# Kernel tuning notes

Measured on AMD Instinct MI355X. Metric: run time of the kernel, lower is better.

Reference implementation:

```python
import jax, jax.numpy as jnp
import numpy as np

B, A, D, H = 16384, 16, 512, 512


def setup_inputs() -> dict:
    key = jax.random.key(0)
    ks = jax.random.split(key, 8)
    s = 1.0 / np.sqrt(D)
    sh = 1.0 / np.sqrt(H)
    return {
        "state": jax.random.normal(ks[0], (B, D), jnp.float32),
        "W1": jax.random.normal(ks[1], (A, D, H), jnp.float32) * s,
        "b1": jax.random.normal(ks[2], (A, H), jnp.float32) * s,
        "W2": jax.random.normal(ks[3], (A, H, H), jnp.float32) * sh,
        "b2": jax.random.normal(ks[4], (A, H), jnp.float32) * sh,
        "W3": jax.random.normal(ks[5], (A, H, 1), jnp.float32) * sh,
        "b3": jax.random.normal(ks[6], (A, 1), jnp.float32) * sh,
        "actions": jax.random.randint(ks[7], (B,), 0, A, jnp.int64),
    }


def reference(state, W1, b1, W2, b2, W3, b3, actions):
    # All per-action MLPs applied to every state as grouped/batched GEMMs.
    # h1, h2: [B, A, H]; out: [B, A, n_out]
    h1 = jax.nn.relu(jnp.einsum("bd,adh->bah", state, W1) + b1)
    h2 = jax.nn.relu(jnp.einsum("bah,ahk->bak", h1, W2) + b2)
    out = jnp.einsum("bah,ahk->bak", h2, W3) + b3  # [B, A, 1]
    # Gather the selected action's output per batch element -> [B, n_out]
    return jnp.take_along_axis(out, actions[:, None, None], axis=1)[:, 0, :]
```

## Files before the change

### kernel.cpp

```cpp
#include <hip/hip_runtime.h>
#include <hip/hip_bf16.h>
#include <stdint.h>

typedef __hip_bfloat16 bf16;
typedef float f32x4 __attribute__((ext_vector_type(4)));
typedef short bf16x8 __attribute__((ext_vector_type(8)));

#define NB 16384
#define NA 16
#define ND 512
#define NH 512
#define TR 80

#define W1S_OFF 0u
#define W2S_OFF 8388608u
#define PERM_OFF 16777216u
#define META_OFF 16842752u

__device__ __forceinline__ unsigned short f2b(float x) {
  unsigned int b = __float_as_uint(x);
  return (unsigned short)((b + 0x7FFFu + ((b >> 16) & 1u)) >> 16);
}

__global__ __launch_bounds__(256) void k_prep(const float* __restrict__ W1,
                                              const float* __restrict__ W2,
                                              bf16* __restrict__ W1s,
                                              bf16* __restrict__ W2s,
                                              const int* __restrict__ act,
                                              int* __restrict__ meta,
                                              int* __restrict__ perm) {
  __shared__ union {
    float tile[2][64][65];
    struct { int hist[16][256]; int off16[16]; } m;
  } lds;
  if (blockIdx.x == 512) {
    int t = threadIdx.x;
    int lane = t & 63, wv = t >> 6;
#pragma unroll
    for (int i = 0; i < 16; ++i) lds.m.hist[i][t] = 0;
    __syncthreads();
    for (int j = 0; j < 64; ++j) {
      int a = act[t + (j << 8)] & 15;
      lds.m.hist[a][t]++;
    }
    __syncthreads();
    for (int q = 0; q < 4; ++q) {
      int a = (wv << 2) + q;
      int base = lane << 2;
      int v0 = lds.m.hist[a][base + 0];
      int v1 = lds.m.hist[a][base + 1];
      int v2 = lds.m.hist[a][base + 2];
      int v3 = lds.m.hist[a][base + 3];
      int s = v0 + v1 + v2 + v3;
      int incl = s;
#pragma unroll
      for (int d = 1; d < 64; d <<= 1) {
        int y = __shfl_up(incl, d);
        if (lane >= d) incl += y;
      }
      int excl = incl - s;
      lds.m.hist[a][base + 0] = excl;
      lds.m.hist[a][base + 1] = excl + v0;
      lds.m.hist[a][base + 2] = excl + v0 + v1;
      lds.m.hist[a][base + 3] = excl + v0 + v1 + v2;
      if (lane == 63) lds.m.off16[a] = incl;
    }
    __syncthreads();
    if (t == 0) {
      int o = 0;
      for (int aa = 0; aa < 16; ++aa) {
        int c = lds.m.off16[aa];
        meta[aa] = c;
        meta[16 + aa] = o;
        lds.m.off16[aa] = o;
        o += c;
      }
    }
    __syncthreads();
    for (int j = 0; j < 64; ++j) {
      int idx = t + (j << 8);
      int a = act[idx] & 15;
      int pos = lds.m.off16[a] + lds.m.hist[a][t]++;
      perm[pos] = idx;
    }
    return;
  }
  int bid = blockIdx.x;
  int xcd = bid & 7, q = bid >> 3;
  int t = threadIdx.x;
  int r0 = t >> 2, c0 = (t & 3) << 4;
  int wv = t >> 6, l = t & 63;
  int l15b = l & 15, l4b = l >> 4;

  float4 v[4];
  char* dstb_r[4];
  int td_r[4], th_r[4];
#pragma unroll
  for (int r = 0; r < 4; ++r) {
    int jj = q + (r << 6);
    int mi = jj >> 6;
    int mat = (mi < 2) ? ((xcd << 1) + mi) : (NA + (xcd << 1) + (mi - 2));
    dstb_r[r] = (mat < NA) ? ((char*)W1s + ((size_t)mat << 19))
                           : ((char*)W2s + ((size_t)(mat - NA) << 19));
    int tl = jj & 63;
    td_r[r] = tl >> 3;
    th_r[r] = tl & 7;
  }
  {
    int mi0 = q >> 6;
    const float* src = W1 + (size_t)((xcd << 1) + mi0) * (ND * NH);
    const float* sp = src + (size_t)(td_r[0] * 64 + r0) * NH + th_r[0] * 64 + c0;
    v[0] = ((const float4*)sp)[0];
    v[1] = ((const float4*)sp)[1];
    v[2] = ((const float4*)sp)[2];
    v[3] = ((const float4*)sp)[3];
  }
#pragma unroll
  for (int r = 0; r < 4; ++r) {
    int buf = r & 1;
    float* trp = &lds.tile[buf][r0][c0];
    trp[0] = v[0].x; trp[1] = v[0].y; trp[2] = v[0].z; trp[3] = v[0].w;
    trp[4] = v[1].x; trp[5] = v[1].y; trp[6] = v[1].z; trp[7] = v[1].w;
    trp[8] = v[2].x; trp[9] = v[2].y; trp[10] = v[2].z; trp[11] = v[2].w;
    trp[12] = v[3].x; trp[13] = v[3].y; trp[14] = v[3].z; trp[15] = v[3].w;
    __syncthreads();
    if (r < 3) {
      int jj = q + ((r + 1) << 6);
      int mi = jj >> 6;
      int mat = (mi < 2) ? ((xcd << 1) + mi) : (NA + (xcd << 1) + (mi - 2));
      const float* src = (mat < NA) ? (W1 + (size_t)mat * (ND * NH))
                                    : (W2 + (size_t)(mat - NA) * (ND * NH));
      const float* sp = src + (size_t)(td_r[r + 1] * 64 + r0) * NH + th_r[r + 1] * 64 + c0;
      v[0] = ((const float4*)sp)[0];
      v[1] = ((const float4*)sp)[1];
      v[2] = ((const float4*)sp)[2];
      v[3] = ((const float4*)sp)[3];
    }
#pragma unroll
    for (int kc = 0; kc < 2; ++kc) {
      union { unsigned short us[8]; uint4 qd; } u;
#pragma unroll
      for (int i = 0; i < 8; ++i)
        u.us[i] = f2b(lds.tile[buf][kc * 32 + l4b * 8 + i][wv * 16 + l15b]);
      int hb = th_r[r] * 4 + wv;
      int kb = td_r[r] * 2 + kc;
      *(uint4*)(dstb_r[r] + ((size_t)(hb * 16 + kb) << 10) + (l << 4)) = u.qd;
    }
  }
}

__global__ __launch_bounds__(1024) void k_main(
    const float* __restrict__ state, const float* __restrict__ b1,
    const float* __restrict__ b2, const float* __restrict__ W3,
    const float* __restrict__ b3, const bf16* __restrict__ W1s,
    const bf16* __restrict__ W2s, const int* __restrict__ perm,
    const int* __restrict__ meta, float* __restrict__ out) {
  extern __shared__ char smem[];
  char* Xs = smem;
  float* outbuf = (float*)(smem + 81920);

  int bid = blockIdx.x;
  int xcd = bid & 7, slot = bid >> 3;
  int a0 = xcd << 1;
  int n0 = meta[a0], n1 = meta[a0 + 1];
  int nt0 = (n0 + TR - 1) / TR, nt1 = (n1 + TR - 1) / TR;
  int a, t;
  if (slot < nt0) {
    a = a0; t = slot;
  } else if (slot < nt0 + nt1) {
    a = a0 + 1; t = slot - nt0;
  } else {
    return;
  }
  int rowbase = meta[16 + a] + t * TR;
  int nrows = meta[a] - t * TR;
  nrows = nrows > TR ? TR : nrows;

  int tid = threadIdx.x;
  int lane = tid & 63;
  int w = tid >> 6;
  int hw = w & 7;
  int ch = w >> 3;
  int bf0 = ch ? 3 : 0;
  int bfn = ch ? 2 : 3;
  int l15 = lane & 15, l4 = lane >> 4;

  const char* Wl = (const char*)W1s + ((size_t)a << 19) + (hw << 16) + (lane << 4);
  const char* Wl2 = (const char*)W2s + ((size_t)a << 19) + (hw << 16) + (lane << 4);

  bf16x8 A[2][4];
  bf16x8 Bc[3];
#pragma unroll
  for (int s = 0; s < 2; ++s)
#pragma unroll
    for (int hf = 0; hf < 4; ++hf)
      A[s][hf] = *(const bf16x8*)(Wl + (hf << 14) + (s << 10));

  {
#pragma unroll
    for (int it = 0; it < 10; ++it) {
      int c = tid + (it << 10);
      int row = c >> 7, chunk = c & 127;
      int gr = (row < nrows) ? perm[rowbase + row] : -1;
      float4 v = make_float4(0.f, 0.f, 0.f, 0.f);
      if (gr >= 0) v = *(const float4*)(state + (size_t)gr * ND + (chunk << 2));
      uint2 pk;
      pk.x = (unsigned)f2b(v.x) | ((unsigned)f2b(v.y) << 16);
      pk.y = (unsigned)f2b(v.z) | ((unsigned)f2b(v.w) << 16);
      *(uint2*)(Xs + row * 1024 + ((chunk << 3) ^ ((row & 7) << 4))) = pk;
    }
  }
  __syncthreads();

  uint2 h1p[12];

  {
    f32x4 acc[4][3] = {};
#pragma unroll
    for (int ks = 0; ks < 16; ++ks) {
#pragma unroll
      for (int bf = 0; bf < 3; ++bf) {
        if (bf < bfn) {
          int b = ((bf0 + bf) << 4) + l15;
          Bc[bf] = *(const bf16x8*)(Xs + b * 1024 + (((ks << 6) + (l4 << 4)) ^ ((b & 7) << 4)));
        }
      }
      __builtin_amdgcn_s_setprio(1);
#pragma unroll
      for (int hf = 0; hf < 4; ++hf)
#pragma unroll
        for (int bf = 0; bf < 3; ++bf)
          if (bf < bfn)
            acc[hf][bf] = __builtin_amdgcn_mfma_f32_16x16x32_bf16(A[ks & 1][hf], Bc[bf], acc[hf][bf], 0, 0, 0);
      __builtin_amdgcn_s_setprio(0);
      if (ks < 14) {
#pragma unroll
        for (int hf = 0; hf < 4; ++hf)
          A[ks & 1][hf] = *(const bf16x8*)(Wl + (hf << 14) + ((ks + 2) << 10));
      }
    }
#pragma unroll
    for (int s = 0; s < 2; ++s)
#pragma unroll
      for (int hf = 0; hf < 4; ++hf)
        A[s][hf] = *(const bf16x8*)(Wl2 + (hf << 14) + (s << 10));
#pragma unroll
    for (int hf = 0; hf < 4; ++hf) {
      int hb = (hw << 6) + (hf << 4) + (l4 << 2);
      float4 bias = *(const float4*)(b1 + (a << 9) + hb);
#pragma unroll
      for (int bf = 0; bf < 3; ++bf) {
        if (bf < bfn) {
          float x0 = fmaxf(acc[hf][bf][0] + bias.x, 0.f);
          float x1 = fmaxf(acc[hf][bf][1] + bias.y, 0.f);
          float x2 = fmaxf(acc[hf][bf][2] + bias.z, 0.f);
          float x3 = fmaxf(acc[hf][bf][3] + bias.w, 0.f);
          h1p[hf * 3 + bf].x = (unsigned)f2b(x0) | ((unsigned)f2b(x1) << 16);
          h1p[hf * 3 + bf].y = (unsigned)f2b(x2) | ((unsigned)f2b(x3) << 16);
        }
      }
    }
  }
  __syncthreads();
#pragma unroll
  for (int hf = 0; hf < 4; ++hf) {
    int hb2 = ((hw << 6) + (hf << 4) + (l4 << 2)) << 1;
#pragma unroll
    for (int bf = 0; bf < 3; ++bf) {
      if (bf < bfn) {
        int b = ((bf0 + bf) << 4) + l15;
        *(uint2*)(Xs + b * 1024 + (hb2 ^ ((b & 7) << 4))) = h1p[hf * 3 + bf];
      }
    }
  }
  __syncthreads();

  {
    f32x4 acc[4][3] = {};
#pragma unroll
    for (int ks = 0; ks < 16; ++ks) {
#pragma unroll
      for (int bf = 0; bf < 3; ++bf) {
        if (bf < bfn) {
          int b = ((bf0 + bf) << 4) + l15;
          Bc[bf] = *(const bf16x8*)(Xs + b * 1024 + (((ks << 6) + (l4 << 4)) ^ ((b & 7) << 4)));
        }
      }
      __builtin_amdgcn_s_setprio(1);
#pragma unroll
      for (int hf = 0; hf < 4; ++hf)
#pragma unroll
        for (int bf = 0; bf < 3; ++bf)
          if (bf < bfn)
            acc[hf][bf] = __builtin_amdgcn_mfma_f32_16x16x32_bf16(A[ks & 1][hf], Bc[bf], acc[hf][bf], 0, 0, 0);
      __builtin_amdgcn_s_setprio(0);
      if (ks < 14) {
#pragma unroll
        for (int hf = 0; hf < 4; ++hf)
          A[ks & 1][hf] = *(const bf16x8*)(Wl2 + (hf << 14) + ((ks + 2) << 10));
      }
    }
    float part[3] = {0.f, 0.f, 0.f};
#pragma unroll
    for (int hf = 0; hf < 4; ++hf) {
      int hb = (hw << 6) + (hf << 4) + (l4 << 2);
      float4 bias = *(const float4*)(b2 + (a << 9) + hb);
      float4 w3v = *(const float4*)(W3 + (a << 9) + hb);
#pragma unroll
      for (int bf = 0; bf < 3; ++bf) {
        if (bf < bfn) {
          part[bf] += fmaxf(acc[hf][bf][0] + bias.x, 0.f) * w3v.x +
                      fmaxf(acc[hf][bf][1] + bias.y, 0.f) * w3v.y +
                      fmaxf(acc[hf][bf][2] + bias.z, 0.f) * w3v.z +
                      fmaxf(acc[hf][bf][3] + bias.w, 0.f) * w3v.w;
        }
      }
    }
#pragma unroll
    for (int bf = 0; bf < 3; ++bf) {
      if (bf < bfn) {
        float p = part[bf];
        p += __shfl_xor(p, 16);
        p += __shfl_xor(p, 32);
        if (l4 == 0) outbuf[w * TR + ((bf0 + bf) << 4) + l15] = p;
      }
    }
  }
  __syncthreads();
  if (tid < nrows) {
    float s = b3[a];
    int wb = (tid < 48) ? 0 : 8;
#pragma unroll
    for (int ww = 0; ww < 8; ++ww) s += outbuf[(wb + ww) * TR + tid];
    out[perm[rowbase + tid]] = s;
  }
}

extern "C" void kernel_launch(void* const* d_in, const int* in_sizes, int n_in,
                              void* d_out, int out_size, void* d_ws, size_t ws_size,
                              hipStream_t stream) {
  const float* state = (const float*)d_in[0];
  const float* W1 = (const float*)d_in[1];
  const float* b1 = (const float*)d_in[2];
  const float* W2 = (const float*)d_in[3];
  const float* b2 = (const float*)d_in[4];
  const float* W3 = (const float*)d_in[5];
  const float* b3 = (const float*)d_in[6];
  const int* actions = (const int*)d_in[7];
  float* out = (float*)d_out;
  char* ws = (char*)d_ws;
  bf16* W1s = (bf16*)(ws + W1S_OFF);
  bf16* W2s = (bf16*)(ws + W2S_OFF);
  int* perm = (int*)(ws + PERM_OFF);
  int* meta = (int*)(ws + META_OFF);

  k_prep<<<513, 256, 0, stream>>>(W1, W2, W1s, W2s, actions, meta, perm);
  hipFuncSetAttribute((const void*)k_main, hipFuncAttributeMaxDynamicSharedMemorySize, 87040);
  k_main<<<256, 1024, 87040, stream>>>(state, b1, b2, W3, b3, W1s, W2s, perm, meta, out);
}
```

Measured before the change: 59.30 us.

## Split weight-prep into one tile per block and hint k_main occupancy

The prep kernel now launches 2048 blocks, one 64x64 tile each, instead of 512 blocks that each loop over four tiles with double-buffered LDS and register prefetch. The aim is more parallel memory traffic and less serial work per block during the fp32-to-bf16 swizzle of W1/W2. Per-block software pipelining goes away and block launch overhead grows. k_main also gets a launch_bounds minimum-blocks hint of 4, which may constrain register allocation.

```diff
diff --git a/kernel.cpp b/kernel.cpp
--- a/kernel.cpp
+++ b/kernel.cpp
@@ -30,10 +30,10 @@
                                               int* __restrict__ meta,
                                               int* __restrict__ perm) {
   __shared__ union {
-    float tile[2][64][65];
+    float tile[64][65];
     struct { int hist[16][256]; int off16[16]; } m;
   } lds;
-  if (blockIdx.x == 512) {
+  if (blockIdx.x == 2048) {
     int t = threadIdx.x;
     int lane = t & 63, wv = t >> 6;
 #pragma unroll
@@ -85,71 +85,43 @@
     }
     return;
   }
-  int bid = blockIdx.x;
-  int xcd = bid & 7, q = bid >> 3;
+  int j = blockIdx.x;
+  int xcd = j & 7;
+  int job = j >> 3;
+  int mi = job >> 6;
+  int m = (mi < 2) ? ((xcd << 1) + mi) : (NA + (xcd << 1) + (mi - 2));
+  int tl = job & 63;
+  int td = tl >> 3, th = tl & 7;
+  const float* src = (m < NA) ? (W1 + (size_t)m * (ND * NH)) : (W2 + (size_t)(m - NA) * (ND * NH));
+  char* dstb = (m < NA) ? ((char*)W1s + ((size_t)m << 19)) : ((char*)W2s + ((size_t)(m - NA) << 19));
   int t = threadIdx.x;
-  int r0 = t >> 2, c0 = (t & 3) << 4;
+  int r = t >> 2, c0 = (t & 3) << 4;
+  const float* sp = src + (size_t)(td * 64 + r) * NH + th * 64 + c0;
+  float4 v0 = ((const float4*)sp)[0];
+  float4 v1 = ((const float4*)sp)[1];
+  float4 v2 = ((const float4*)sp)[2];
+  float4 v3 = ((const float4*)sp)[3];
+  float* tr = &lds.tile[r][c0];
+  tr[0] = v0.x; tr[1] = v0.y; tr[2] = v0.z; tr[3] = v0.w;
+  tr[4] = v1.x; tr[5] = v1.y; tr[6] = v1.z; tr[7] = v1.w;
+  tr[8] = v2.x; tr[9] = v2.y; tr[10] = v2.z; tr[11] = v2.w;
+  tr[12] = v3.x; tr[13] = v3.y; tr[14] = v3.z; tr[15] = v3.w;
+  __syncthreads();
   int wv = t >> 6, l = t & 63;
   int l15b = l & 15, l4b = l >> 4;
-
-  float4 v[4];
-  char* dstb_r[4];
-  int td_r[4], th_r[4];
-#pragma unroll
-  for (int r = 0; r < 4; ++r) {
-    int jj = q + (r << 6);
-    int mi = jj >> 6;
-    int mat = (mi < 2) ? ((xcd << 1) + mi) : (NA + (xcd << 1) + (mi - 2));
-    dstb_r[r] = (mat < NA) ? ((char*)W1s + ((size_t)mat << 19))
-                           : ((char*)W2s + ((size_t)(mat - NA) << 19));
-    int tl = jj & 63;
-    td_r[r] = tl >> 3;
-    th_r[r] = tl & 7;
-  }
-  {
-    int mi0 = q >> 6;
-    const float* src = W1 + (size_t)((xcd << 1) + mi0) * (ND * NH);
-    const float* sp = src + (size_t)(td_r[0] * 64 + r0) * NH + th_r[0] * 64 + c0;
-    v[0] = ((const float4*)sp)[0];
-    v[1] = ((const float4*)sp)[1];
-    v[2] = ((const float4*)sp)[2];
-    v[3] = ((const float4*)sp)[3];
-  }
-#pragma unroll
-  for (int r = 0; r < 4; ++r) {
-    int buf = r & 1;
-    float* trp = &lds.tile[buf][r0][c0];
-    trp[0] = v[0].x; trp[1] = v[0].y; trp[2] = v[0].z; trp[3] = v[0].w;
-    trp[4] = v[1].x; trp[5] = v[1].y; trp[6] = v[1].z; trp[7] = v[1].w;
-    trp[8] = v[2].x; trp[9] = v[2].y; trp[10] = v[2].z; trp[11] = v[2].w;
-    trp[12] = v[3].x; trp[13] = v[3].y; trp[14] = v[3].z; trp[15] = v[3].w;
-    __syncthreads();
-    if (r < 3) {
-      int jj = q + ((r + 1) << 6);
-      int mi = jj >> 6;
-      int mat = (mi < 2) ? ((xcd << 1) + mi) : (NA + (xcd << 1) + (mi - 2));
-      const float* src = (mat < NA) ? (W1 + (size_t)mat * (ND * NH))
-                                    : (W2 + (size_t)(mat - NA) * (ND * NH));
-      const float* sp = src + (size_t)(td_r[r + 1] * 64 + r0) * NH + th_r[r + 1] * 64 + c0;
-      v[0] = ((const float4*)sp)[0];
-      v[1] = ((const float4*)sp)[1];
-      v[2] = ((const float4*)sp)[2];
-      v[3] = ((const float4*)sp)[3];
-    }
-#pragma unroll
-    for (int kc = 0; kc < 2; ++kc) {
-      union { unsigned short us[8]; uint4 qd; } u;
-#pragma unroll
-      for (int i = 0; i < 8; ++i)
-        u.us[i] = f2b(lds.tile[buf][kc * 32 + l4b * 8 + i][wv * 16 + l15b]);
-      int hb = th_r[r] * 4 + wv;
-      int kb = td_r[r] * 2 + kc;
-      *(uint4*)(dstb_r[r] + ((size_t)(hb * 16 + kb) << 10) + (l << 4)) = u.qd;
-    }
+#pragma unroll
+  for (int kc = 0; kc < 2; ++kc) {
+    union { unsigned short us[8]; uint4 q; } u;
+#pragma unroll
+    for (int i = 0; i < 8; ++i)
+      u.us[i] = f2b(lds.tile[kc * 32 + l4b * 8 + i][wv * 16 + l15b]);
+    int hb = th * 4 + wv;
+    int kb = td * 2 + kc;
+    *(uint4*)(dstb + ((size_t)(hb * 16 + kb) << 10) + (l << 4)) = u.q;
   }
 }
 
-__global__ __launch_bounds__(1024) void k_main(
+__global__ __launch_bounds__(1024, 4) void k_main(
     const float* __restrict__ state, const float* __restrict__ b1,
     const float* __restrict__ b2, const float* __restrict__ W3,
     const float* __restrict__ b3, const bf16* __restrict__ W1s,
@@ -354,7 +326,7 @@
   int* perm = (int*)(ws + PERM_OFF);
   int* meta = (int*)(ws + META_OFF);
 
-  k_prep<<<513, 256, 0, stream>>>(W1, W2, W1s, W2s, actions, meta, perm);
+  k_prep<<<2049, 256, 0, stream>>>(W1, W2, W1s, W2s, actions, meta, perm);
   hipFuncSetAttribute((const void*)k_main, hipFuncAttributeMaxDynamicSharedMemorySize, 87040);
   k_main<<<256, 1024, 87040, stream>>>(state, b1, b2, W3, b3, W1s, W2s, perm, meta, out);
 }
```

New measurement: 59.57 us. No clear change (+0.5%).
